# Kernel tuning notes

Hardware: AMD Instinct MI355X
Metric: run time of the kernel (lower is better)

Reference implementation:

```python
import jax, jax.numpy as jnp
import numpy as np

EMBED = 1024
MLP = 2048
N_EXPERTS = 8
TOP_K = 2


def setup_inputs() -> dict:
    key = jax.random.key(0)
    ks = jax.random.split(key, 5)
    scale_e = 1.0 / np.sqrt(EMBED)
    scale_m = 1.0 / np.sqrt(MLP)
    x = jax.random.normal(ks[0], (4, 2048, EMBED), dtype=jnp.float32)
    gate_w = jax.random.normal(ks[1], (EMBED, N_EXPERTS), dtype=jnp.float32) * scale_e
    w1 = jax.random.normal(ks[2], (N_EXPERTS, EMBED, MLP), dtype=jnp.float32) * scale_e
    w3 = jax.random.normal(ks[3], (N_EXPERTS, EMBED, MLP), dtype=jnp.float32) * scale_e
    w2 = jax.random.normal(ks[4], (N_EXPERTS, MLP, EMBED), dtype=jnp.float32) * scale_m
    return {"x": x, "gate_w": gate_w, "w1": w1, "w2": w2, "w3": w3}


def reference(x, gate_w, w1, w2, w3):
    B, S, D = x.shape
    xf = x.reshape(-1, D)  # [T, D] tokens
    # Router: softmax over experts, top-k select, renormalize selected weights
    router_logits = xf @ gate_w                      # [T, E]
    routing_weights = jax.nn.softmax(router_logits, axis=-1)
    sel_w, sel_e = jax.lax.top_k(routing_weights, TOP_K)  # [T, K]
    sel_w = sel_w / jnp.sum(sel_w, axis=-1, keepdims=True)
    out = jnp.zeros_like(xf)
    # Loop over the small fixed expert set; tokens not routed to expert e get
    # coefficient 0, matching the gather/scatter-add combine of the original.
    for e in range(N_EXPERTS):
        coef = jnp.sum(jnp.where(sel_e == e, sel_w, 0.0), axis=-1)  # [T]
        h = jax.nn.silu(xf @ w1[e]) * (xf @ w3[e])                  # [T, Mlp] SwiGLU
        out = out + coef[:, None] * (h @ w2[e])                     # [T, D]
    return out.reshape(B, S, D)
```

## Files before the change

### kernel.cpp

```cpp
#include <hip/hip_runtime.h>

#define EMBED 1024
#define MLP   2048
#define NE    8
#define NTOK  8192
#define RMAX  (2*NTOK + NE*128)
#define BK    64

typedef _Float16 f16x8 __attribute__((ext_vector_type(8)));
typedef _Float16 f16x4 __attribute__((ext_vector_type(4)));
typedef float    f32x4 __attribute__((ext_vector_type(4)));

__device__ __forceinline__ void async_copy16(const void* g, void* l) {
  __builtin_amdgcn_global_load_lds(
      (const __attribute__((address_space(1))) unsigned int*)g,
      (__attribute__((address_space(3))) unsigned int*)l, 16, 0, 0);
}

__global__ __launch_bounds__(256) void router_kernel(
    const float* __restrict__ x, const float* __restrict__ gw,
    int* __restrict__ sel_e, float* __restrict__ sel_w, int* __restrict__ counts)
{
  __shared__ float gwt[NE * EMBED];
  __shared__ int cnt[NE];
  int tid = threadIdx.x;
  for (int idx = tid; idx < NE * EMBED; idx += 256) {
    int i = idx >> 3, e = idx & 7;
    gwt[e * EMBED + i] = gw[idx];
  }
  if (tid < NE) cnt[tid] = 0;
  __syncthreads();

  int lane = tid & 63, wv = tid >> 6;
  int t = blockIdx.x * 4 + wv;
  const float4* xr = (const float4*)(x + (size_t)t * EMBED);
  const float4* gt4 = (const float4*)gwt;
  float acc[NE];
  #pragma unroll
  for (int e = 0; e < NE; ++e) acc[e] = 0.f;
  #pragma unroll
  for (int c = 0; c < 4; ++c) {
    float4 xv = xr[c * 64 + lane];
    #pragma unroll
    for (int e = 0; e < NE; ++e) {
      float4 gv = gt4[e * 256 + c * 64 + lane];
      acc[e] += xv.x * gv.x + xv.y * gv.y + xv.z * gv.z + xv.w * gv.w;
    }
  }
  #pragma unroll
  for (int off = 1; off < 64; off <<= 1) {
    #pragma unroll
    for (int e = 0; e < NE; ++e) acc[e] += __shfl_xor(acc[e], off);
  }
  if (lane == 0) {
    int e0 = 0; float l0 = acc[0];
    #pragma unroll
    for (int e = 1; e < NE; ++e) if (acc[e] > l0) { l0 = acc[e]; e0 = e; }
    int e1 = -1; float l1 = -1e30f;
    #pragma unroll
    for (int e = 0; e < NE; ++e) if (e != e0 && acc[e] > l1) { l1 = acc[e]; e1 = e; }
    float w0 = 1.f / (1.f + expf(l1 - l0));
    sel_e[2 * t] = e0;     sel_w[2 * t] = w0;
    sel_e[2 * t + 1] = e1; sel_w[2 * t + 1] = 1.f - w0;
    atomicAdd(&cnt[e0], 1); atomicAdd(&cnt[e1], 1);
  }
  __syncthreads();
  if (tid < NE && cnt[tid]) atomicAdd(&counts[tid], cnt[tid]);
}

__global__ void offsets_kernel(const int* __restrict__ counts,
                               int* __restrict__ offs, int* __restrict__ cursor)
{
  if (threadIdx.x == 0) {
    int o = 0;
    for (int e = 0; e < NE; ++e) {
      offs[e] = o; cursor[e] = o;
      o += (counts[e] + 127) & ~127;
    }
    offs[NE] = o;
  }
}

__global__ __launch_bounds__(256) void assign_kernel(
    const int* __restrict__ sel_e, const float* __restrict__ sel_w,
    int* __restrict__ cursor, int* __restrict__ rowtok, float* __restrict__ rowcoef,
    int* __restrict__ inv)
{
  int t = blockIdx.x * 256 + threadIdx.x;
  int lane = threadIdx.x & 63;
  #pragma unroll
  for (int k = 0; k < 2; ++k) {
    int e = sel_e[2 * t + k];
    float w = sel_w[2 * t + k];
    for (int xch = 0; xch < NE; ++xch) {
      unsigned long long m = __ballot(e == xch);
      if (e == xch) {
        int leader = __ffsll((unsigned long long)m) - 1;
        int base = 0;
        if (lane == leader) base = atomicAdd(&cursor[xch], (int)__popcll(m));
        base = __shfl(base, leader);
        int pos = base + (int)__popcll(m & ((1ull << lane) - 1));
        rowtok[pos] = t;
        rowcoef[pos] = w;
        inv[2 * t + k] = pos;
      }
    }
  }
}

__global__ __launch_bounds__(256) void gather_kernel(
    const float* __restrict__ x, const int* __restrict__ rowtok,
    _Float16* __restrict__ xg)
{
  int r = blockIdx.x;
  int tok = rowtok[r];
  int t4 = threadIdx.x * 4;
  _Float16* dst = xg + (size_t)r * EMBED + t4;
  if (tok >= 0) {
    float4 v = *(const float4*)(x + (size_t)tok * EMBED + t4);
    f16x4 h; h.x = (_Float16)v.x; h.y = (_Float16)v.y; h.z = (_Float16)v.z; h.w = (_Float16)v.w;
    *(f16x4*)dst = h;
  } else {
    f16x4 z = {(_Float16)0.f, (_Float16)0.f, (_Float16)0.f, (_Float16)0.f};
    *(f16x4*)dst = z;
  }
}

__global__ __launch_bounds__(256) void transpose_all_kernel(
    const float* __restrict__ w1, const float* __restrict__ w3,
    const float* __restrict__ w2, _Float16* __restrict__ w1t,
    _Float16* __restrict__ w3t, _Float16* __restrict__ w2t)
{
  int id = blockIdx.x;
  int mat = id >> 12;
  int rr = id & 4095;
  int e = rr >> 9, tile = rr & 511;
  const float* src; _Float16* dst; int K, N;
  if (mat == 0)      { src = w1; dst = w1t; K = EMBED; N = MLP; }
  else if (mat == 1) { src = w3; dst = w3t; K = EMBED; N = MLP; }
  else               { src = w2; dst = w2t; K = MLP;   N = EMBED; }
  int nx = K >> 6;
  int k0 = (tile % nx) * 64, n0 = (tile / nx) * 64;
  src += (size_t)e * K * N;
  dst += (size_t)e * K * N;

  __shared__ float tilebuf[64][65];
  int t = threadIdx.x;
  int r = t >> 4, c4 = (t & 15) * 4;
  #pragma unroll
  for (int i = 0; i < 4; ++i) {
    float4 v = *(const float4*)(src + (size_t)(k0 + r + 16 * i) * N + n0 + c4);
    tilebuf[r + 16 * i][c4 + 0] = v.x;
    tilebuf[r + 16 * i][c4 + 1] = v.y;
    tilebuf[r + 16 * i][c4 + 2] = v.z;
    tilebuf[r + 16 * i][c4 + 3] = v.w;
  }
  __syncthreads();
  int kk8 = (t & 7) * 8, nIdx = t >> 3;
  #pragma unroll
  for (int i = 0; i < 2; ++i) {
    int n = nIdx + 32 * i;
    f16x8 h;
    #pragma unroll
    for (int j = 0; j < 8; ++j) h[j] = (_Float16)tilebuf[kk8 + j][n];
    *(f16x8*)(dst + (size_t)(n0 + n) * K + k0 + kk8) = h;
  }
}

__device__ __forceinline__ int resolve_expert(const int* __restrict__ offs, int r0)
{
  int e = 0;
  #pragma unroll
  for (int q = 0; q < NE - 1; ++q) if (r0 >= offs[q + 1]) e = q + 1;
  return e;
}

__device__ __forceinline__ const _Float16* bfrag_addr(const _Float16* buf, int row,
                                                      int s, int quad)
{
  return buf + row * BK + ((((s << 2) + quad) ^ (row & 7)) << 3);
}

__global__ __launch_bounds__(256, 2) void gemm1_kernel(
    const _Float16* __restrict__ xg, const _Float16* __restrict__ w1t,
    const _Float16* __restrict__ w3t, const float* __restrict__ rowcoef,
    const int* __restrict__ offs, _Float16* __restrict__ hb)
{
  int r0 = blockIdx.x * 128;
  if (r0 >= offs[NE]) return;
  int e = resolve_expert(offs, r0);
  int n0 = blockIdx.y * 128;
  const _Float16* B1 = w1t + (size_t)e * MLP * EMBED;
  const _Float16* B3 = w3t + (size_t)e * MLP * EMBED;

  __shared__ __align__(16) _Float16 Bs1[128 * BK];
  __shared__ __align__(16) _Float16 Bs3[128 * BK];

  int tid = threadIdx.x, lane = tid & 63, wv = tid >> 6;
  int wm = (wv & 1) << 6, wn = (wv >> 1) << 6;
  int l16 = lane & 15, quad = lane >> 4;

  const _Float16* Arow[4];
  #pragma unroll
  for (int i = 0; i < 4; ++i)
    Arow[i] = xg + (size_t)(r0 + wm + 16 * i + l16) * EMBED + quad * 8;

  f32x4 acc1[4][4], acc3[4][4];
  f32x4 z4 = {0.f, 0.f, 0.f, 0.f};
  #pragma unroll
  for (int i = 0; i < 4; ++i)
    #pragma unroll
    for (int j = 0; j < 4; ++j) { acc1[i][j] = z4; acc3[i][j] = z4; }

  for (int kk = 0; kk < EMBED; kk += BK) {
    __syncthreads();
    #pragma unroll
    for (int p = 0; p < 4; ++p) {
      int c = p * 256 + tid;
      int row = c >> 3, cp = c & 7;
      int cl = cp ^ (row & 7);
      size_t gof = (size_t)(n0 + row) * EMBED + kk + cl * 8;
      int lof = (p * 256 + wv * 64) * 8;
      async_copy16(B1 + gof, Bs1 + lof);
      async_copy16(B3 + gof, Bs3 + lof);
    }
    f16x8 af[2][4];
    #pragma unroll
    for (int s = 0; s < 2; ++s)
      #pragma unroll
      for (int i = 0; i < 4; ++i)
        af[s][i] = *(const f16x8*)(Arow[i] + kk + s * 32);
    __syncthreads();
    #pragma unroll
    for (int s = 0; s < 2; ++s) {
      f16x8 b1f[4], b3f[4];
      #pragma unroll
      for (int j = 0; j < 4; ++j) {
        int row = wn + 16 * j + l16;
        b1f[j] = *(const f16x8*)bfrag_addr(Bs1, row, s, quad);
        b3f[j] = *(const f16x8*)bfrag_addr(Bs3, row, s, quad);
      }
      #pragma unroll
      for (int i = 0; i < 4; ++i)
        #pragma unroll
        for (int j = 0; j < 4; ++j) {
          acc1[i][j] = __builtin_amdgcn_mfma_f32_16x16x32_f16(af[s][i], b1f[j], acc1[i][j], 0, 0, 0);
          acc3[i][j] = __builtin_amdgcn_mfma_f32_16x16x32_f16(af[s][i], b3f[j], acc3[i][j], 0, 0, 0);
        }
    }
  }

  #pragma unroll
  for (int i = 0; i < 4; ++i) {
    int mb = r0 + wm + 16 * i + quad * 4;
    float cf[4];
    #pragma unroll
    for (int rg = 0; rg < 4; ++rg) cf[rg] = rowcoef[mb + rg];
    #pragma unroll
    for (int j = 0; j < 4; ++j) {
      int col = n0 + wn + 16 * j + l16;
      #pragma unroll
      for (int rg = 0; rg < 4; ++rg) {
        float g = acc1[i][j][rg], u = acc3[i][j][rg];
        float h = g * u * cf[rg] / (1.f + __expf(-g));
        hb[(size_t)(mb + rg) * MLP + col] = (_Float16)h;
      }
    }
  }
}

__global__ __launch_bounds__(256, 2) void gemm2_kernel(
    const _Float16* __restrict__ hb, const _Float16* __restrict__ w2t,
    const int* __restrict__ offs, _Float16* __restrict__ hb2)
{
  int r0 = blockIdx.x * 128;
  if (r0 >= offs[NE]) return;
  int e = resolve_expert(offs, r0);
  int n0 = blockIdx.y * 128;
  const _Float16* B = w2t + (size_t)e * EMBED * MLP;

  __shared__ __align__(16) _Float16 Bs[128 * BK];

  int tid = threadIdx.x, lane = tid & 63, wv = tid >> 6;
  int wm = (wv & 1) << 6, wn = (wv >> 1) << 6;
  int l16 = lane & 15, quad = lane >> 4;

  const _Float16* Arow[4];
  #pragma unroll
  for (int i = 0; i < 4; ++i)
    Arow[i] = hb + (size_t)(r0 + wm + 16 * i + l16) * MLP + quad * 8;

  f32x4 acc[4][4];
  f32x4 z4 = {0.f, 0.f, 0.f, 0.f};
  #pragma unroll
  for (int i = 0; i < 4; ++i)
    #pragma unroll
    for (int j = 0; j < 4; ++j) acc[i][j] = z4;

  for (int kk = 0; kk < MLP; kk += BK) {
    __syncthreads();
    #pragma unroll
    for (int p = 0; p < 4; ++p) {
      int c = p * 256 + tid;
      int row = c >> 3, cp = c & 7;
      int cl = cp ^ (row & 7);
      size_t gof = (size_t)(n0 + row) * MLP + kk + cl * 8;
      int lof = (p * 256 + wv * 64) * 8;
      async_copy16(B + gof, Bs + lof);
    }
    f16x8 af[2][4];
    #pragma unroll
    for (int s = 0; s < 2; ++s)
      #pragma unroll
      for (int i = 0; i < 4; ++i)
        af[s][i] = *(const f16x8*)(Arow[i] + kk + s * 32);
    __syncthreads();
    #pragma unroll
    for (int s = 0; s < 2; ++s) {
      f16x8 bf[4];
      #pragma unroll
      for (int j = 0; j < 4; ++j)
        bf[j] = *(const f16x8*)bfrag_addr(Bs, wn + 16 * j + l16, s, quad);
      #pragma unroll
      for (int i = 0; i < 4; ++i)
        #pragma unroll
        for (int j = 0; j < 4; ++j)
          acc[i][j] = __builtin_amdgcn_mfma_f32_16x16x32_f16(af[s][i], bf[j], acc[i][j], 0, 0, 0);
    }
  }

  #pragma unroll
  for (int i = 0; i < 4; ++i) {
    int mb = r0 + wm + 16 * i + quad * 4;
    #pragma unroll
    for (int j = 0; j < 4; ++j) {
      int col = n0 + wn + 16 * j + l16;
      #pragma unroll
      for (int rg = 0; rg < 4; ++rg)
        hb2[(size_t)(mb + rg) * EMBED + col] = (_Float16)acc[i][j][rg];
    }
  }
}

__global__ __launch_bounds__(256) void combine_kernel(
    const _Float16* __restrict__ hb2, const int* __restrict__ inv,
    float* __restrict__ out)
{
  int t = blockIdx.x;
  int d = threadIdx.x * 4;
  int p0 = inv[2 * t], p1 = inv[2 * t + 1];
  f16x4 a = *(const f16x4*)(hb2 + (size_t)p0 * EMBED + d);
  f16x4 b = *(const f16x4*)(hb2 + (size_t)p1 * EMBED + d);
  float4 r;
  r.x = (float)a.x + (float)b.x;
  r.y = (float)a.y + (float)b.y;
  r.z = (float)a.z + (float)b.z;
  r.w = (float)a.w + (float)b.w;
  *(float4*)(out + (size_t)t * EMBED + d) = r;
}

extern "C" void kernel_launch(void* const* d_in, const int* in_sizes, int n_in,
                              void* d_out, int out_size, void* d_ws, size_t ws_size,
                              hipStream_t stream)
{
  (void)in_sizes; (void)n_in; (void)ws_size; (void)out_size;
  const float* x  = (const float*)d_in[0];
  const float* gw = (const float*)d_in[1];
  const float* w1 = (const float*)d_in[2];
  const float* w2 = (const float*)d_in[3];
  const float* w3 = (const float*)d_in[4];
  float* out = (float*)d_out;
  char* ws = (char*)d_ws;

  size_t o = 0;
  auto alloc = [&](size_t bytes) { size_t r = o; o = (o + bytes + 255) & ~255ULL; return r; };
  const size_t wbytes = (size_t)NE * MLP * EMBED * 2;
  _Float16* w1t = (_Float16*)(ws + alloc(wbytes));
  _Float16* w3t = (_Float16*)(ws + alloc(wbytes));
  _Float16* w2t = (_Float16*)(ws + alloc(wbytes));
  _Float16* xg  = (_Float16*)(ws + alloc((size_t)RMAX * EMBED * 2));
  _Float16* hb  = (_Float16*)(ws + alloc((size_t)RMAX * MLP * 2));
  int*   rowtok  = (int*)(ws + alloc((size_t)RMAX * 4));
  float* rowcoef = (float*)(ws + alloc((size_t)RMAX * 4));
  int*   sel_e   = (int*)(ws + alloc((size_t)2 * NTOK * 4));
  float* sel_w   = (float*)(ws + alloc((size_t)2 * NTOK * 4));
  int*   inv     = (int*)(ws + alloc((size_t)2 * NTOK * 4));
  int*   meta    = (int*)(ws + alloc(256));
  int* counts = meta;
  int* offs   = meta + 8;
  int* cursor = meta + 17;
  _Float16* hb2 = xg;

  hipMemsetAsync(meta, 0, 256, stream);
  hipMemsetAsync(rowtok, 0xFF, (size_t)RMAX * 4, stream);
  hipMemsetAsync(rowcoef, 0, (size_t)RMAX * 4, stream);

  transpose_all_kernel<<<3 * 4096, 256, 0, stream>>>(w1, w3, w2, w1t, w3t, w2t);

  router_kernel<<<NTOK / 4, 256, 0, stream>>>(x, gw, sel_e, sel_w, counts);
  offsets_kernel<<<1, 64, 0, stream>>>(counts, offs, cursor);
  assign_kernel<<<NTOK / 256, 256, 0, stream>>>(sel_e, sel_w, cursor, rowtok, rowcoef, inv);
  gather_kernel<<<RMAX, 256, 0, stream>>>(x, rowtok, xg);

  gemm1_kernel<<<dim3(RMAX / 128, MLP / 128), 256, 0, stream>>>(xg, w1t, w3t, rowcoef, offs, hb);
  gemm2_kernel<<<dim3(RMAX / 128, EMBED / 128), 256, 0, stream>>>(hb, w2t, offs, hb2);
  combine_kernel<<<NTOK, 256, 0, stream>>>(hb2, inv, out);
}
```

Before: 709.6 us.

## Triple-buffer A and B tiles via async LDS loads in expert GEMMs

Both expert GEMMs now stage the activation tile as well as the weight tile into LDS with async global-to-LDS copies, using a 3-deep ring buffer of BK=32 slices. Each iteration issues the next stage, waits on vmcnt, and uses a single barrier, so memory latency can overlap with MFMA work. Previously A fragments came straight from global memory and there were two syncthreads per step. The separate offsets kernel is folded into assign_kernel, which computes the expert offsets per thread, dropping one launch. The deeper pipeline raises LDS use, which may limit occupancy, and the single barrier with 3 buffers depends on the vmcnt accounting being correct.

```diff
diff --git a/kernel.cpp b/kernel.cpp
--- a/kernel.cpp
+++ b/kernel.cpp
@@ -5,7 +5,6 @@
 #define NE    8
 #define NTOK  8192
 #define RMAX  (2*NTOK + NE*128)
-#define BK    64
 
 typedef _Float16 f16x8 __attribute__((ext_vector_type(8)));
 typedef _Float16 f16x4 __attribute__((ext_vector_type(4)));
@@ -68,24 +67,23 @@
   if (tid < NE && cnt[tid]) atomicAdd(&counts[tid], cnt[tid]);
 }
 
-__global__ void offsets_kernel(const int* __restrict__ counts,
-                               int* __restrict__ offs, int* __restrict__ cursor)
-{
-  if (threadIdx.x == 0) {
-    int o = 0;
-    for (int e = 0; e < NE; ++e) {
-      offs[e] = o; cursor[e] = o;
-      o += (counts[e] + 127) & ~127;
-    }
-    offs[NE] = o;
-  }
-}
-
 __global__ __launch_bounds__(256) void assign_kernel(
     const int* __restrict__ sel_e, const float* __restrict__ sel_w,
-    int* __restrict__ cursor, int* __restrict__ rowtok, float* __restrict__ rowcoef,
-    int* __restrict__ inv)
-{
+    const int* __restrict__ counts, int* __restrict__ cursor,
+    int* __restrict__ offs_out, int* __restrict__ rowtok,
+    float* __restrict__ rowcoef, int* __restrict__ inv)
+{
+  int offl[NE];
+  {
+    int o = 0;
+    #pragma unroll
+    for (int e = 0; e < NE; ++e) { offl[e] = o; o += (counts[e] + 127) & ~127; }
+    if (blockIdx.x == 0 && threadIdx.x == 0) {
+      #pragma unroll
+      for (int e = 0; e < NE; ++e) offs_out[e] = offl[e];
+      offs_out[NE] = o;
+    }
+  }
   int t = blockIdx.x * 256 + threadIdx.x;
   int lane = threadIdx.x & 63;
   #pragma unroll
@@ -99,7 +97,7 @@
         int base = 0;
         if (lane == leader) base = atomicAdd(&cursor[xch], (int)__popcll(m));
         base = __shfl(base, leader);
-        int pos = base + (int)__popcll(m & ((1ull << lane) - 1));
+        int pos = offl[xch] + base + (int)__popcll(m & ((1ull << lane) - 1));
         rowtok[pos] = t;
         rowcoef[pos] = w;
         inv[2 * t + k] = pos;
@@ -175,10 +173,9 @@
   return e;
 }
 
-__device__ __forceinline__ const _Float16* bfrag_addr(const _Float16* buf, int row,
-                                                      int s, int quad)
-{
-  return buf + row * BK + ((((s << 2) + quad) ^ (row & 7)) << 3);
+__device__ __forceinline__ const _Float16* frag_addr(const _Float16* buf, int row, int quad)
+{
+  return buf + row * 32 + ((quad ^ ((row >> 1) & 3)) << 3);
 }
 
 __global__ __launch_bounds__(256, 2) void gemm1_kernel(
@@ -193,17 +190,24 @@
   const _Float16* B1 = w1t + (size_t)e * MLP * EMBED;
   const _Float16* B3 = w3t + (size_t)e * MLP * EMBED;
 
-  __shared__ __align__(16) _Float16 Bs1[128 * BK];
-  __shared__ __align__(16) _Float16 Bs3[128 * BK];
+  __shared__ __align__(16) _Float16 As[3][128 * 32];
+  __shared__ __align__(16) _Float16 Bs1[3][128 * 32];
+  __shared__ __align__(16) _Float16 Bs3[3][128 * 32];
 
   int tid = threadIdx.x, lane = tid & 63, wv = tid >> 6;
   int wm = (wv & 1) << 6, wn = (wv >> 1) << 6;
   int l16 = lane & 15, quad = lane >> 4;
 
-  const _Float16* Arow[4];
-  #pragma unroll
-  for (int i = 0; i < 4; ++i)
-    Arow[i] = xg + (size_t)(r0 + wm + 16 * i + l16) * EMBED + quad * 8;
+  int row0 = tid >> 2,        kqp0 = tid & 3;
+  int row1 = (256 + tid) >> 2, kqp1 = tid & 3;
+  int kql0 = kqp0 ^ ((row0 >> 1) & 3);
+  int kql1 = kqp1 ^ ((row1 >> 1) & 3);
+  size_t gA0 = (size_t)(r0 + row0) * EMBED + kql0 * 8;
+  size_t gA1 = (size_t)(r0 + row1) * EMBED + kql1 * 8;
+  size_t gB0 = (size_t)(n0 + row0) * EMBED + kql0 * 8;
+  size_t gB1 = (size_t)(n0 + row1) * EMBED + kql1 * 8;
+  int lof0 = (wv * 64) * 8;
+  int lof1 = (256 + wv * 64) * 8;
 
   f32x4 acc1[4][4], acc3[4][4];
   f32x4 z4 = {0.f, 0.f, 0.f, 0.f};
@@ -212,42 +216,43 @@
     #pragma unroll
     for (int j = 0; j < 4; ++j) { acc1[i][j] = z4; acc3[i][j] = z4; }
 
-  for (int kk = 0; kk < EMBED; kk += BK) {
-    __syncthreads();
-    #pragma unroll
-    for (int p = 0; p < 4; ++p) {
-      int c = p * 256 + tid;
-      int row = c >> 3, cp = c & 7;
-      int cl = cp ^ (row & 7);
-      size_t gof = (size_t)(n0 + row) * EMBED + kk + cl * 8;
-      int lof = (p * 256 + wv * 64) * 8;
-      async_copy16(B1 + gof, Bs1 + lof);
-      async_copy16(B3 + gof, Bs3 + lof);
-    }
-    f16x8 af[2][4];
-    #pragma unroll
-    for (int s = 0; s < 2; ++s)
-      #pragma unroll
-      for (int i = 0; i < 4; ++i)
-        af[s][i] = *(const f16x8*)(Arow[i] + kk + s * 32);
-    __syncthreads();
-    #pragma unroll
-    for (int s = 0; s < 2; ++s) {
-      f16x8 b1f[4], b3f[4];
+  auto stage = [&](int b, int kk) {
+    async_copy16(xg + gA0 + kk, &As[b][lof0]);
+    async_copy16(B1 + gB0 + kk, &Bs1[b][lof0]);
+    async_copy16(B3 + gB0 + kk, &Bs3[b][lof0]);
+    async_copy16(xg + gA1 + kk, &As[b][lof1]);
+    async_copy16(B1 + gB1 + kk, &Bs1[b][lof1]);
+    async_copy16(B3 + gB1 + kk, &Bs3[b][lof1]);
+  };
+
+  const int NIT = EMBED / 32;
+  stage(0, 0);
+  for (int k = 0; k < NIT; ++k) {
+    int b = k % 3;
+    if (k + 1 < NIT) {
+      stage((k + 1) % 3, (k + 1) * 32);
+      asm volatile("s_waitcnt vmcnt(6)" ::: "memory");
+    } else {
+      asm volatile("s_waitcnt vmcnt(0)" ::: "memory");
+    }
+    asm volatile("s_barrier" ::: "memory");
+
+    f16x8 af[4], b1f[4], b3f[4];
+    #pragma unroll
+    for (int i = 0; i < 4; ++i)
+      af[i] = *(const f16x8*)frag_addr(As[b], wm + 16 * i + l16, quad);
+    #pragma unroll
+    for (int j = 0; j < 4; ++j) {
+      b1f[j] = *(const f16x8*)frag_addr(Bs1[b], wn + 16 * j + l16, quad);
+      b3f[j] = *(const f16x8*)frag_addr(Bs3[b], wn + 16 * j + l16, quad);
+    }
+    #pragma unroll
+    for (int i = 0; i < 4; ++i)
       #pragma unroll
       for (int j = 0; j < 4; ++j) {
-        int row = wn + 16 * j + l16;
-        b1f[j] = *(const f16x8*)bfrag_addr(Bs1, row, s, quad);
-        b3f[j] = *(const f16x8*)bfrag_addr(Bs3, row, s, quad);
+        acc1[i][j] = __builtin_amdgcn_mfma_f32_16x16x32_f16(af[i], b1f[j], acc1[i][j], 0, 0, 0);
+        acc3[i][j] = __builtin_amdgcn_mfma_f32_16x16x32_f16(af[i], b3f[j], acc3[i][j], 0, 0, 0);
       }
-      #pragma unroll
-      for (int i = 0; i < 4; ++i)
-        #pragma unroll
-        for (int j = 0; j < 4; ++j) {
-          acc1[i][j] = __builtin_amdgcn_mfma_f32_16x16x32_f16(af[s][i], b1f[j], acc1[i][j], 0, 0, 0);
-          acc3[i][j] = __builtin_amdgcn_mfma_f32_16x16x32_f16(af[s][i], b3f[j], acc3[i][j], 0, 0, 0);
-        }
-    }
   }
 
   #pragma unroll
@@ -279,16 +284,23 @@
   int n0 = blockIdx.y * 128;
   const _Float16* B = w2t + (size_t)e * EMBED * MLP;
 
-  __shared__ __align__(16) _Float16 Bs[128 * BK];
+  __shared__ __align__(16) _Float16 As[3][128 * 32];
+  __shared__ __align__(16) _Float16 Bs[3][128 * 32];
 
   int tid = threadIdx.x, lane = tid & 63, wv = tid >> 6;
   int wm = (wv & 1) << 6, wn = (wv >> 1) << 6;
   int l16 = lane & 15, quad = lane >> 4;
 
-  const _Float16* Arow[4];
-  #pragma unroll
-  for (int i = 0; i < 4; ++i)
-    Arow[i] = hb + (size_t)(r0 + wm + 16 * i + l16) * MLP + quad * 8;
+  int row0 = tid >> 2,        kqp0 = tid & 3;
+  int row1 = (256 + tid) >> 2, kqp1 = tid & 3;
+  int kql0 = kqp0 ^ ((row0 >> 1) & 3);
+  int kql1 = kqp1 ^ ((row1 >> 1) & 3);
+  size_t gA0 = (size_t)(r0 + row0) * MLP + kql0 * 8;
+  size_t gA1 = (size_t)(r0 + row1) * MLP + kql1 * 8;
+  size_t gB0 = (size_t)(n0 + row0) * MLP + kql0 * 8;
+  size_t gB1 = (size_t)(n0 + row1) * MLP + kql1 * 8;
+  int lof0 = (wv * 64) * 8;
+  int lof1 = (256 + wv * 64) * 8;
 
   f32x4 acc[4][4];
   f32x4 z4 = {0.f, 0.f, 0.f, 0.f};
@@ -297,36 +309,37 @@
     #pragma unroll
     for (int j = 0; j < 4; ++j) acc[i][j] = z4;
 
-  for (int kk = 0; kk < MLP; kk += BK) {
-    __syncthreads();
-    #pragma unroll
-    for (int p = 0; p < 4; ++p) {
-      int c = p * 256 + tid;
-      int row = c >> 3, cp = c & 7;
-      int cl = cp ^ (row & 7);
-      size_t gof = (size_t)(n0 + row) * MLP + kk + cl * 8;
-      int lof = (p * 256 + wv * 64) * 8;
-      async_copy16(B + gof, Bs + lof);
-    }
-    f16x8 af[2][4];
-    #pragma unroll
-    for (int s = 0; s < 2; ++s)
-      #pragma unroll
-      for (int i = 0; i < 4; ++i)
-        af[s][i] = *(const f16x8*)(Arow[i] + kk + s * 32);
-    __syncthreads();
-    #pragma unroll
-    for (int s = 0; s < 2; ++s) {
-      f16x8 bf[4];
+  auto stage = [&](int b, int kk) {
+    async_copy16(hb + gA0 + kk, &As[b][lof0]);
+    async_copy16(B  + gB0 + kk, &Bs[b][lof0]);
+    async_copy16(hb + gA1 + kk, &As[b][lof1]);
+    async_copy16(B  + gB1 + kk, &Bs[b][lof1]);
+  };
+
+  const int NIT = MLP / 32;
+  stage(0, 0);
+  for (int k = 0; k < NIT; ++k) {
+    int b = k % 3;
+    if (k + 1 < NIT) {
+      stage((k + 1) % 3, (k + 1) * 32);
+      asm volatile("s_waitcnt vmcnt(4)" ::: "memory");
+    } else {
+      asm volatile("s_waitcnt vmcnt(0)" ::: "memory");
+    }
+    asm volatile("s_barrier" ::: "memory");
+
+    f16x8 af[4], bf[4];
+    #pragma unroll
+    for (int i = 0; i < 4; ++i)
+      af[i] = *(const f16x8*)frag_addr(As[b], wm + 16 * i + l16, quad);
+    #pragma unroll
+    for (int j = 0; j < 4; ++j)
+      bf[j] = *(const f16x8*)frag_addr(Bs[b], wn + 16 * j + l16, quad);
+    #pragma unroll
+    for (int i = 0; i < 4; ++i)
       #pragma unroll
       for (int j = 0; j < 4; ++j)
-        bf[j] = *(const f16x8*)bfrag_addr(Bs, wn + 16 * j + l16, s, quad);
-      #pragma unroll
-      for (int i = 0; i < 4; ++i)
-        #pragma unroll
-        for (int j = 0; j < 4; ++j)
-          acc[i][j] = __builtin_amdgcn_mfma_f32_16x16x32_f16(af[s][i], bf[j], acc[i][j], 0, 0, 0);
-    }
+        acc[i][j] = __builtin_amdgcn_mfma_f32_16x16x32_f16(af[i], bf[j], acc[i][j], 0, 0, 0);
   }
 
   #pragma unroll
@@ -398,8 +411,8 @@
   transpose_all_kernel<<<3 * 4096, 256, 0, stream>>>(w1, w3, w2, w1t, w3t, w2t);
 
   router_kernel<<<NTOK / 4, 256, 0, stream>>>(x, gw, sel_e, sel_w, counts);
-  offsets_kernel<<<1, 64, 0, stream>>>(counts, offs, cursor);
-  assign_kernel<<<NTOK / 256, 256, 0, stream>>>(sel_e, sel_w, cursor, rowtok, rowcoef, inv);
+  assign_kernel<<<NTOK / 256, 256, 0, stream>>>(sel_e, sel_w, counts, cursor,
+                                                offs, rowtok, rowcoef, inv);
   gather_kernel<<<RMAX, 256, 0, stream>>>(x, rowtok, xg);
 
   gemm1_kernel<<<dim3(RMAX / 128, MLP / 128), 256, 0, stream>>>(xg, w1t, w3t, rowcoef, offs, hb);
```

Measured after the change: 637.2 us. 1.11x faster.
